# Kernel optimization log

Measured on AMD Instinct MI355X. Metric: run time of the kernel, lower is better.

## Reference

```python
import jax, jax.numpy as jnp
import numpy as np

N_KERNELS = 21
N_LAYERS = 2
N_HEADS = 8
ATT_DIM = 32
FF_HID = 100
EMB = 300


def kernel_mus(n):
    mus = [1.0]
    bin_size = 2.0 / (n - 1)
    mus.append(1.0 - bin_size / 2.0)
    for _ in range(1, n - 1):
        mus.append(mus[-1] - bin_size)
    return np.array(mus, dtype=np.float32)


def kernel_sigmas(n):
    return np.array([0.001] + [0.1] * (n - 1), dtype=np.float32)


def setup_inputs() -> dict:
    key = jax.random.key(0)
    ks = jax.random.split(key, 12)
    B, LQ, LD = 32, 64, 512
    u = lambda k, s, a: jax.random.uniform(k, s, jnp.float32, -a, a)
    return dict(
        q_embed=jax.random.normal(ks[0], (B, LQ, EMB), jnp.float32),
        d_embed=jax.random.normal(ks[1], (B, LD, EMB), jnp.float32),
        mask_q=(jax.random.uniform(ks[2], (B, LQ)) > 0.1).astype(jnp.float32),
        mask_d=(jax.random.uniform(ks[3], (B, LD)) > 0.1).astype(jnp.float32),
        mixer=jnp.full((1, 1, 1), 0.5, jnp.float32),
        nn_scaler=jnp.full((1,), 0.01, jnp.float32),
        ff_w1=u(ks[4], (N_LAYERS, EMB, FF_HID), 0.05),
        ff_b1=jnp.zeros((N_LAYERS, FF_HID), jnp.float32),
        ff_w2=u(ks[5], (N_LAYERS, FF_HID, EMB), 0.05),
        ff_b2=jnp.zeros((N_LAYERS, EMB), jnp.float32),
        ln1_g=jnp.ones((N_LAYERS, EMB), jnp.float32),
        ln1_b=jnp.zeros((N_LAYERS, EMB), jnp.float32),
        att_w=u(ks[6], (N_LAYERS, EMB, 3 * ATT_DIM), 0.05),
        att_b=jnp.zeros((N_LAYERS, 3 * ATT_DIM), jnp.float32),
        out_w=u(ks[7], (N_LAYERS, ATT_DIM, EMB), 0.05),
        out_b=jnp.zeros((N_LAYERS, EMB), jnp.float32),
        ln2_g=jnp.ones((N_LAYERS, EMB), jnp.float32),
        ln2_b=jnp.zeros((N_LAYERS, EMB), jnp.float32),
        dense_w=u(ks[8], (1, N_KERNELS), 0.014),
    )


def _layer_norm(x, g, b, eps=1e-6):
    m = jnp.mean(x, -1, keepdims=True)
    s = jnp.std(x, -1, keepdims=True, ddof=1)  # torch std is unbiased
    return g * (x - m) / (s + eps) + b


def _encoder(x, mask, p):
    # AllenNLP StackedSelfAttentionEncoder: [FF -> res+LN -> MHSA -> res+LN] x2
    B, T, E = x.shape
    scale = jnp.sqrt(jnp.float32(E // N_HEADS))
    hd = ATT_DIM // N_HEADS
    for l in range(N_LAYERS):
        h = jax.nn.relu(x @ p['ff_w1'][l] + p['ff_b1'][l]) @ p['ff_w2'][l] + p['ff_b2'][l]
        h = _layer_norm(h + x, p['ln1_g'][l], p['ln1_b'][l])
        c = h @ p['att_w'][l] + p['att_b'][l]              # [B,T,3*ATT_DIM]
        q = c[..., :ATT_DIM].reshape(B, T, N_HEADS, hd)
        k = c[..., ATT_DIM:2 * ATT_DIM].reshape(B, T, N_HEADS, hd)
        v = c[..., 2 * ATT_DIM:].reshape(B, T, N_HEADS, hd)
        sims = jnp.einsum('bqhd,bkhd->bhqk', q / scale, k)
        m = mask[:, None, None, :]
        att = jax.nn.softmax(sims * m, axis=-1) * m         # AllenNLP masked_softmax
        att = att / (jnp.sum(att, -1, keepdims=True) + 1e-13)
        o = jnp.einsum('bhqk,bkhd->bqhd', att, v).reshape(B, T, ATT_DIM)
        o = o @ p['out_w'][l] + p['out_b'][l]
        x = _layer_norm(o + h, p['ln2_g'][l], p['ln2_b'][l])
    return x


def reference(q_embed, d_embed, mask_q, mask_d, mixer, nn_scaler,
              ff_w1, ff_b1, ff_w2, ff_b2, ln1_g, ln1_b,
              att_w, att_b, out_w, out_b, ln2_g, ln2_b, dense_w):
    p = dict(ff_w1=ff_w1, ff_b1=ff_b1, ff_w2=ff_w2, ff_b2=ff_b2,
             ln1_g=ln1_g, ln1_b=ln1_b, att_w=att_w, att_b=att_b,
             out_w=out_w, out_b=out_b, ln2_g=ln2_g, ln2_b=ln2_b)
    mu = jnp.asarray(kernel_mus(N_KERNELS))        # [K]
    sigma = jnp.asarray(kernel_sigmas(N_KERNELS))  # [K]
    mq = mask_q[..., None]
    md = mask_d[..., None]
    q = q_embed * mq
    d = d_embed * md
    qc = _encoder(q, mask_q, p)
    dc = _encoder(d, mask_d, p)
    q = (mixer * q + (1.0 - mixer) * qc) * mq
    d = (mixer * d + (1.0 - mixer) * dc) * md
    qd_mask = mask_q[:, :, None] * mask_d[:, None, :]  # [B,Q,D]
    qn = q / (jnp.linalg.norm(q, axis=-1, keepdims=True) + 1e-13)
    dn = d / (jnp.linalg.norm(d, axis=-1, keepdims=True) + 1e-13)
    cos = jnp.einsum('bqe,bde->bqd', qn, dn) * qd_mask
    # Gaussian RBF soft histogram: [B,Q,D,K]
    kr = jnp.exp(-(cos[..., None] - mu) ** 2 / (2.0 * sigma ** 2)) * qd_mask[..., None]
    pkq = jnp.sum(kr, axis=2)                                 # [B,Q,K]
    log_pkq = jnp.log2(jnp.clip(pkq, 1e-10)) * nn_scaler
    per_kernel = jnp.sum(log_pkq * mq, axis=1)                # [B,K]
    return jnp.squeeze(per_kernel @ dense_w.T, axis=1)        # [B]
```

## Files before the change

### kernel.cpp

```cpp
#include <hip/hip_runtime.h>
#include <hip/hip_bf16.h>

#define BATCH 32
#define LQ 64
#define LD 512
#define EMB 300
#define FFH 100
#define ATTD 32
#define NH 8
#define NK 21
#define MQ (BATCH * LQ)
#define MD (BATCH * LD)
#define MALL (MQ + MD)

typedef __attribute__((ext_vector_type(8))) short bf16x8;
typedef __attribute__((ext_vector_type(4))) float f32x4;

__device__ __forceinline__ float wave_sum(float v) {
    #pragma unroll
    for (int off = 32; off > 0; off >>= 1) v += __shfl_xor(v, off);
    return v;
}

__device__ __forceinline__ float bf2f(__hip_bfloat16 h) {
    return __bfloat162float(h);
}

__device__ __forceinline__ float4 bf4_to_f4(const __hip_bfloat16* p) {
    uint2 u = *(const uint2*)p;
    float4 f;
    f.x = __uint_as_float((u.x & 0xffffu) << 16);
    f.y = __uint_as_float(u.x & 0xffff0000u);
    f.z = __uint_as_float((u.y & 0xffffu) << 16);
    f.w = __uint_as_float(u.y & 0xffff0000u);
    return f;
}

__global__ void maskmul_all(const float* __restrict__ q_embed, const float* __restrict__ d_embed,
                            const float* __restrict__ mask_q, const float* __restrict__ mask_d,
                            __hip_bfloat16* __restrict__ xbf, float* __restrict__ mall) {
    int i = blockIdx.x * blockDim.x + threadIdx.x;
    if (i >= MALL * EMB) return;
    int tok = i / EMB;
    float m, v;
    if (tok < MQ) {
        m = mask_q[tok];
        v = q_embed[i];
    } else {
        m = mask_d[tok - MQ];
        v = d_embed[i - MQ * EMB];
    }
    xbf[i] = __float2bfloat16(v * m);
    if (i % EMB == 0) mall[tok] = m;
}

__device__ __forceinline__ void conv_seg(const float* __restrict__ w, __hip_bfloat16* __restrict__ wt,
                                         int j, int K, int N) {
    int l = j / (K * N);
    int r = j % (K * N);
    int k = r / N, n = r % N;
    wt[(size_t)l * N * K + (size_t)n * K + k] = __float2bfloat16(w[j]);
}
__global__ void convert_all(const float* __restrict__ w1, const float* __restrict__ w2,
                            const float* __restrict__ aw, const float* __restrict__ ow,
                            __hip_bfloat16* __restrict__ w1t, __hip_bfloat16* __restrict__ w2t,
                            __hip_bfloat16* __restrict__ awt, __hip_bfloat16* __restrict__ owt) {
    int i = blockIdx.x * blockDim.x + threadIdx.x;
    const int S1 = 2 * EMB * FFH;
    const int S2 = S1 + 2 * FFH * EMB;
    const int S3 = S2 + 2 * EMB * 96;
    const int S4 = S3 + 2 * ATTD * EMB;
    if (i < S1)       conv_seg(w1, w1t, i, EMB, FFH);
    else if (i < S2)  conv_seg(w2, w2t, i - S1, FFH, EMB);
    else if (i < S3)  conv_seg(aw, awt, i - S2, EMB, 96);
    else if (i < S4)  conv_seg(ow, owt, i - S3, ATTD, EMB);
}

__device__ __forceinline__ void stage_row8(const __hip_bfloat16* __restrict__ src, bool rowvalid,
                                           int K, int gk, __hip_bfloat16* dst) {
    if (rowvalid && gk + 8 <= K) {
        const uint2* p = (const uint2*)(src + gk);
        uint2 a = p[0], b = p[1];
        *(uint2*)dst = a;
        *(uint2*)(dst + 4) = b;
    } else {
        #pragma unroll
        for (int j = 0; j < 8; j++)
            dst[j] = (rowvalid && gk + j < K) ? src[gk + j] : __float2bfloat16(0.f);
    }
}

template <bool RELU, bool HAS_RES>
__global__ __launch_bounds__(256) void gemm_mfma(const __hip_bfloat16* __restrict__ A,
                                                 const __hip_bfloat16* __restrict__ Bt,
                                                 const float* __restrict__ bias,
                                                 const __hip_bfloat16* __restrict__ Rres,
                                                 __hip_bfloat16* __restrict__ Cb,
                                                 int M, int N, int K) {
    __shared__ __align__(16) __hip_bfloat16 As[64][40];
    __shared__ __align__(16) __hip_bfloat16 Bs[64][40];
    const int tid = threadIdx.x;
    const int m0 = blockIdx.y * 64, n0 = blockIdx.x * 64;
    const int lane = tid & 63;
    const int wv = tid >> 6;
    const int wm = wv >> 1, wn = wv & 1;
    const int l15 = lane & 15, lg = lane >> 4;
    const int srow = tid >> 2, sk8 = (tid & 3) * 8;
    f32x4 acc[2][2] = {};
    const int NS = (K + 31) >> 5;
    const __hip_bfloat16* arow = A + (size_t)(m0 + srow) * K;
    const bool bvalid = (n0 + srow) < N;
    const __hip_bfloat16* brow = Bt + (size_t)(n0 + srow) * K;

    for (int s = 0; s < NS; s++) {
        const int gk = (s << 5) + sk8;
        if (s) __syncthreads();
        stage_row8(arow, true, K, gk, &As[srow][sk8]);
        stage_row8(brow, bvalid, K, gk, &Bs[srow][sk8]);
        __syncthreads();
        bf16x8 af0 = *(const bf16x8*)&As[wm * 32 + l15][lg * 8];
        bf16x8 af1 = *(const bf16x8*)&As[wm * 32 + 16 + l15][lg * 8];
        bf16x8 bf0 = *(const bf16x8*)&Bs[wn * 32 + l15][lg * 8];
        bf16x8 bf1 = *(const bf16x8*)&Bs[wn * 32 + 16 + l15][lg * 8];
        acc[0][0] = __builtin_amdgcn_mfma_f32_16x16x32_bf16(af0, bf0, acc[0][0], 0, 0, 0);
        acc[0][1] = __builtin_amdgcn_mfma_f32_16x16x32_bf16(af0, bf1, acc[0][1], 0, 0, 0);
        acc[1][0] = __builtin_amdgcn_mfma_f32_16x16x32_bf16(af1, bf0, acc[1][0], 0, 0, 0);
        acc[1][1] = __builtin_amdgcn_mfma_f32_16x16x32_bf16(af1, bf1, acc[1][1], 0, 0, 0);
    }

    #pragma unroll
    for (int fc = 0; fc < 2; fc++) {
        int col = n0 + wn * 32 + fc * 16 + l15;
        if (col >= N) continue;
        float bs = bias[col];
        #pragma unroll
        for (int fr = 0; fr < 2; fr++) {
            int rbase = m0 + wm * 32 + fr * 16 + lg * 4;
            #pragma unroll
            for (int r = 0; r < 4; r++) {
                int row = rbase + r;
                float v = acc[fr][fc][r] + bs;
                if (RELU) v = fmaxf(v, 0.f);
                size_t idx = (size_t)row * N + col;
                if (HAS_RES) v += bf2f(Rres[idx]);
                Cb[idx] = __float2bfloat16(v);
            }
        }
    }
}

__global__ __launch_bounds__(256) void cos_mfma(const __hip_bfloat16* __restrict__ Qn,
                                                const __hip_bfloat16* __restrict__ Dn,
                                                float* __restrict__ Cos) {
    __shared__ __align__(16) __hip_bfloat16 As[64][40];
    __shared__ __align__(16) __hip_bfloat16 Bs[64][40];
    const int b = blockIdx.y;
    const int n0 = blockIdx.x * 64;
    const int tid = threadIdx.x;
    const int lane = tid & 63;
    const int wv = tid >> 6;
    const int wm = wv >> 1, wn = wv & 1;
    const int l15 = lane & 15, lg = lane >> 4;
    const int srow = tid >> 2, sk8 = (tid & 3) * 8;
    f32x4 acc[2][2] = {};
    const int NS = (EMB + 31) >> 5;
    const __hip_bfloat16* arow = Qn + ((size_t)b * LQ + srow) * EMB;
    const __hip_bfloat16* brow = Dn + ((size_t)b * LD + n0 + srow) * EMB;

    for (int s = 0; s < NS; s++) {
        const int gk = (s << 5) + sk8;
        if (s) __syncthreads();
        stage_row8(arow, true, EMB, gk, &As[srow][sk8]);
        stage_row8(brow, true, EMB, gk, &Bs[srow][sk8]);
        __syncthreads();
        bf16x8 af0 = *(const bf16x8*)&As[wm * 32 + l15][lg * 8];
        bf16x8 af1 = *(const bf16x8*)&As[wm * 32 + 16 + l15][lg * 8];
        bf16x8 bf0 = *(const bf16x8*)&Bs[wn * 32 + l15][lg * 8];
        bf16x8 bf1 = *(const bf16x8*)&Bs[wn * 32 + 16 + l15][lg * 8];
        acc[0][0] = __builtin_amdgcn_mfma_f32_16x16x32_bf16(af0, bf0, acc[0][0], 0, 0, 0);
        acc[0][1] = __builtin_amdgcn_mfma_f32_16x16x32_bf16(af0, bf1, acc[0][1], 0, 0, 0);
        acc[1][0] = __builtin_amdgcn_mfma_f32_16x16x32_bf16(af1, bf0, acc[1][0], 0, 0, 0);
        acc[1][1] = __builtin_amdgcn_mfma_f32_16x16x32_bf16(af1, bf1, acc[1][1], 0, 0, 0);
    }

    float* cb = Cos + (size_t)b * LQ * LD;
    #pragma unroll
    for (int fc = 0; fc < 2; fc++) {
        int col = n0 + wn * 32 + fc * 16 + l15;
        #pragma unroll
        for (int fr = 0; fr < 2; fr++) {
            int rbase = wm * 32 + fr * 16 + lg * 4;
            #pragma unroll
            for (int r = 0; r < 4; r++) {
                cb[(size_t)(rbase + r) * LD + col] = acc[fr][fc][r];
            }
        }
    }
}

__global__ __launch_bounds__(256) void ln_bf(const __hip_bfloat16* __restrict__ X,
                                             const float* __restrict__ g,
                                             const float* __restrict__ bta,
                                             __hip_bfloat16* __restrict__ Y, int M) {
    int wid = (blockIdx.x * 256 + threadIdx.x) >> 6;
    int lane = threadIdx.x & 63;
    if (wid >= M) return;
    const __hip_bfloat16* x = X + (size_t)wid * EMB;
    float v[5];
    float s = 0.f;
    #pragma unroll
    for (int r = 0; r < 5; r++) {
        int idx = lane + r * 64;
        float val = (idx < EMB) ? bf2f(x[idx]) : 0.f;
        v[r] = val;
        s += val;
    }
    s = wave_sum(s);
    float mean = s * (1.f / EMB);
    float s2 = 0.f;
    #pragma unroll
    for (int r = 0; r < 5; r++) {
        int idx = lane + r * 64;
        if (idx < EMB) { float d = v[r] - mean; s2 += d * d; }
    }
    s2 = wave_sum(s2);
    float stdv = sqrtf(s2 * (1.f / (EMB - 1)));
    float inv = 1.f / (stdv + 1e-6f);
    __hip_bfloat16* y = Y + (size_t)wid * EMB;
    #pragma unroll
    for (int r = 0; r < 5; r++) {
        int idx = lane + r * 64;
        if (idx < EMB) y[idx] = __float2bfloat16(g[idx] * (v[r] - mean) * inv + bta[idx]);
    }
}

template <int T, int RPB, int KS>
__global__ __launch_bounds__(512) void attn_fused(const __hip_bfloat16* __restrict__ c,
                                                  const float* __restrict__ mask,
                                                  __hip_bfloat16* __restrict__ o32) {
    constexpr int BLK = RPB * KS;
    constexpr int NRB = T / RPB;
    __shared__ float4 Ks[T];
    __shared__ float4 Vs[T];
    __shared__ float part[RPB * 5 * (KS - 1)];
    __shared__ float nmask_s;
    const int bh = blockIdx.x / NRB;
    const int rb = blockIdx.x % NRB;
    const int b = bh / NH, h = bh % NH;
    const int tid = threadIdx.x;
    const __hip_bfloat16* base = c + (size_t)b * T * 96;

    if (tid == 0) nmask_s = 0.f;
    __syncthreads();
    float lnm = 0.f;
    for (int j = tid; j < T; j += BLK) {
        float m = mask[b * T + j];
        float4 kv = bf4_to_f4(base + (size_t)j * 96 + ATTD + h * 4);
        float4 vv = bf4_to_f4(base + (size_t)j * 96 + 2 * ATTD + h * 4);
        kv.x *= m; kv.y *= m; kv.z *= m; kv.w *= m;
        vv.x *= m; vv.y *= m; vv.z *= m; vv.w *= m;
        Ks[j] = kv;
        Vs[j] = vv;
        lnm += 1.f - m;
    }
    lnm = wave_sum(lnm);
    if ((tid & 63) == 0 && lnm != 0.f) atomicAdd(&nmask_s, lnm);
    __syncthreads();

    const int r = rb * RPB + (tid % RPB);
    const int ks = tid / RPB;
    const float inv_scale = 0.16439898730535729f;
    float4 qv = bf4_to_f4(base + (size_t)r * 96 + h * 4);
    qv.x *= inv_scale; qv.y *= inv_scale; qv.z *= inv_scale; qv.w *= inv_scale;

    float Sall = 0.f, ox = 0.f, oy = 0.f, oz = 0.f, ow = 0.f;
    constexpr int KC = T / KS;
    const int k0 = ks * KC;
    #pragma unroll 4
    for (int k = k0; k < k0 + KC; k++) {
        float4 kv = Ks[k];
        float4 vv = Vs[k];
        float s = fmaf(qv.x, kv.x, fmaf(qv.y, kv.y, fmaf(qv.z, kv.z, qv.w * kv.w)));
        float e = __expf(s);
        Sall += e;
        ox = fmaf(e, vv.x, ox);
        oy = fmaf(e, vv.y, oy);
        oz = fmaf(e, vv.z, oz);
        ow = fmaf(e, vv.w, ow);
    }
    if (ks > 0) {
        float* p = &part[((ks - 1) * RPB + (tid % RPB)) * 5];
        p[0] = Sall; p[1] = ox; p[2] = oy; p[3] = oz; p[4] = ow;
    }
    __syncthreads();
    if (ks == 0) {
        #pragma unroll
        for (int s2 = 0; s2 < KS - 1; s2++) {
            const float* p = &part[(s2 * RPB + r - rb * RPB) * 5];
            Sall += p[0]; ox += p[1]; oy += p[2]; oz += p[3]; ow += p[4];
        }
        float Sm = Sall - nmask_s;
        float inv = 1.f / (Sm + 1e-13f * Sall);
        __hip_bfloat16* op = o32 + (size_t)(b * T + r) * ATTD + h * 4;
        op[0] = __float2bfloat16(ox * inv);
        op[1] = __float2bfloat16(oy * inv);
        op[2] = __float2bfloat16(oz * inv);
        op[3] = __float2bfloat16(ow * inv);
    }
}

__global__ __launch_bounds__(256) void mixnorm_bf(const __hip_bfloat16* __restrict__ x,
                                                  const __hip_bfloat16* __restrict__ xc,
                                                  const float* __restrict__ mask,
                                                  const float* __restrict__ mixer,
                                                  __hip_bfloat16* __restrict__ out) {
    int wid = (blockIdx.x * 256 + threadIdx.x) >> 6;
    int lane = threadIdx.x & 63;
    float mixv = mixer[0];
    float mval = mask[wid];
    const __hip_bfloat16* xr = x + (size_t)wid * EMB;
    const __hip_bfloat16* xcr = xc + (size_t)wid * EMB;
    float v[5];
    float s2 = 0.f;
    #pragma unroll
    for (int r = 0; r < 5; r++) {
        int idx = lane + r * 64;
        float val = 0.f;
        if (idx < EMB) val = (mixv * bf2f(xr[idx]) + (1.f - mixv) * bf2f(xcr[idx])) * mval;
        v[r] = val;
        s2 += val * val;
    }
    s2 = wave_sum(s2);
    float inv = 1.f / (sqrtf(s2) + 1e-13f);
    __hip_bfloat16* o = out + (size_t)wid * EMB;
    #pragma unroll
    for (int r = 0; r < 5; r++) {
        int idx = lane + r * 64;
        if (idx < EMB) o[idx] = __float2bfloat16(v[r] * inv);
    }
}

__global__ __launch_bounds__(256) void pool_kernel(const float* __restrict__ Cos,
                                                   const float* __restrict__ mask_q,
                                                   const float* __restrict__ mask_d,
                                                   const float* __restrict__ nn_scaler,
                                                   float* __restrict__ lp) {
    int wid = (blockIdx.x * 256 + threadIdx.x) >> 6;
    int lane = threadIdx.x & 63;
    int b = wid >> 6, qi = wid & 63;
    const float* crow = Cos + ((size_t)b * LQ + qi) * LD;
    const float* md = mask_d + b * LD;
    float acc[NK];
    #pragma unroll
    for (int k = 0; k < NK; k++) acc[k] = 0.f;
    #pragma unroll
    for (int rr = 0; rr < LD / 64; rr++) {
        int dj = rr * 64 + lane;
        float m = md[dj];
        if (m != 0.f) {
            float cv = crow[dj];
            float d0 = cv - 1.0f;
            acc[0] += __expf(d0 * d0 * -500000.0f);
            #pragma unroll
            for (int g = 0; g < 4; g++) {
                float mu_a = 0.95f - 0.5f * g;
                float dc = cv - mu_a;
                float t = __expf(dc * dc * -50.0f);
                float r = __expf(fmaf(-10.0f, dc, -0.5f));
                #pragma unroll
                for (int j = 0; j < 5; j++) {
                    acc[1 + 5 * g + j] += t;
                    t *= r;
                    r *= 0.36787944117144233f;
                }
            }
        }
    }
    float mq = mask_q[b * LQ + qi];
    float ns = nn_scaler[0];
    #pragma unroll
    for (int k = 0; k < NK; k++) {
        float s = wave_sum(acc[k]);
        if (lane == 0) lp[((size_t)b * LQ + qi) * NK + k] = log2f(fmaxf(s, 1e-10f)) * ns * mq;
    }
}

__global__ void final_kernel(const float* __restrict__ lp, const float* __restrict__ dense_w,
                             float* __restrict__ out) {
    int b = blockIdx.x;
    int t = threadIdx.x;
    float s = 0.f;
    if (t < NK) {
        for (int qi = 0; qi < LQ; qi++) s += lp[((size_t)b * LQ + qi) * NK + t];
        s *= dense_w[t];
    }
    s = wave_sum(s);
    if (t == 0) out[b] = s;
}

extern "C" void kernel_launch(void* const* d_in, const int* in_sizes, int n_in,
                              void* d_out, int out_size, void* d_ws, size_t ws_size,
                              hipStream_t stream) {
    (void)in_sizes; (void)n_in; (void)out_size; (void)ws_size;
    const float* q_embed  = (const float*)d_in[0];
    const float* d_embed  = (const float*)d_in[1];
    const float* mask_q   = (const float*)d_in[2];
    const float* mask_d   = (const float*)d_in[3];
    const float* mixer    = (const float*)d_in[4];
    const float* nn_scaler= (const float*)d_in[5];
    const float* ff_w1    = (const float*)d_in[6];
    const float* ff_b1    = (const float*)d_in[7];
    const float* ff_w2    = (const float*)d_in[8];
    const float* ff_b2    = (const float*)d_in[9];
    const float* ln1_g    = (const float*)d_in[10];
    const float* ln1_b    = (const float*)d_in[11];
    const float* att_w    = (const float*)d_in[12];
    const float* att_b    = (const float*)d_in[13];
    const float* out_w    = (const float*)d_in[14];
    const float* out_b    = (const float*)d_in[15];
    const float* ln2_g    = (const float*)d_in[16];
    const float* ln2_b    = (const float*)d_in[17];
    const float* dense_w  = (const float*)d_in[18];
    float* out = (float*)d_out;

    float* ws   = (float*)d_ws;
    float* cosb = ws;
    float* lp   = cosb + 1048576;
    float* mall = lp + 43008;
    __hip_bfloat16* xbf   = (__hip_bfloat16*)(mall + MALL);
    __hip_bfloat16* xcbf  = xbf  + (size_t)MALL * EMB;
    __hip_bfloat16* xc2bf = xcbf + (size_t)MALL * EMB;
    __hip_bfloat16* t2bf  = xc2bf + (size_t)MALL * EMB;
    __hip_bfloat16* hbf   = t2bf + (size_t)MALL * EMB;
    __hip_bfloat16* t1bf  = hbf  + (size_t)MALL * EMB;
    __hip_bfloat16* cbf   = t1bf + (size_t)MALL * FFH;
    __hip_bfloat16* o32bf = cbf  + (size_t)MALL * 96;
    __hip_bfloat16* w1t   = o32bf + (size_t)MALL * ATTD;
    __hip_bfloat16* w2t   = w1t + 2 * FFH * EMB;
    __hip_bfloat16* awt   = w2t + 2 * EMB * FFH;
    __hip_bfloat16* owt   = awt + 2 * 96 * EMB;

    convert_all<<<(196800 + 255) / 256, 256, 0, stream>>>(ff_w1, ff_w2, att_w, out_w,
                                                          w1t, w2t, awt, owt);
    maskmul_all<<<(MALL * EMB + 255) / 256, 256, 0, stream>>>(q_embed, d_embed, mask_q, mask_d,
                                                              xbf, mall);

    const __hip_bfloat16* xcur = xbf;
    for (int l = 0; l < 2; l++) {
        __hip_bfloat16* xout = (l == 0) ? xcbf : xc2bf;
        gemm_mfma<true, false><<<dim3(2, MALL / 64), 256, 0, stream>>>(
            xcur, w1t + (size_t)l * FFH * EMB, ff_b1 + l * FFH, nullptr,
            t1bf, MALL, FFH, EMB);
        gemm_mfma<false, true><<<dim3(5, MALL / 64), 256, 0, stream>>>(
            t1bf, w2t + (size_t)l * EMB * FFH, ff_b2 + l * EMB, xcur,
            t2bf, MALL, EMB, FFH);
        ln_bf<<<MALL / 4, 256, 0, stream>>>(t2bf, ln1_g + l * EMB, ln1_b + l * EMB, hbf, MALL);
        gemm_mfma<false, false><<<dim3(2, MALL / 64), 256, 0, stream>>>(
            hbf, awt + (size_t)l * 96 * EMB, att_b + l * 96, nullptr,
            cbf, MALL, 96, EMB);
        attn_fused<LQ, 64, 8><<<BATCH * NH, 512, 0, stream>>>(cbf, mask_q, o32bf);
        attn_fused<LD, 128, 4><<<BATCH * NH * (LD / 128), 512, 0, stream>>>(
            cbf + (size_t)MQ * 96, mask_d, o32bf + (size_t)MQ * ATTD);
        gemm_mfma<false, true><<<dim3(5, MALL / 64), 256, 0, stream>>>(
            o32bf, owt + (size_t)l * EMB * ATTD, out_b + l * EMB, hbf,
            t2bf, MALL, EMB, ATTD);
        ln_bf<<<MALL / 4, 256, 0, stream>>>(t2bf, ln2_g + l * EMB, ln2_b + l * EMB, xout, MALL);
        xcur = xout;
    }

    mixnorm_bf<<<MALL / 4, 256, 0, stream>>>(xbf, xc2bf, mall, mixer, hbf);

    cos_mfma<<<dim3(LD / 64, BATCH), 256, 0, stream>>>(hbf, hbf + (size_t)MQ * EMB, cosb);

    pool_kernel<<<(BATCH * LQ) / 4, 256, 0, stream>>>(cosb, mask_q, mask_d, nn_scaler, lp);

    final_kernel<<<BATCH, 64, 0, stream>>>(lp, dense_w, out);
}
```

Baseline: 242.8 us.

## Fuse residual+LayerNorm into full-row GEMM epilogue and merge attention launches

```diff
diff --git a/kernel.cpp b/kernel.cpp
--- a/kernel.cpp
+++ b/kernel.cpp
@@ -90,11 +90,10 @@
     }
 }
 
-template <bool RELU, bool HAS_RES>
+template <bool RELU>
 __global__ __launch_bounds__(256) void gemm_mfma(const __hip_bfloat16* __restrict__ A,
                                                  const __hip_bfloat16* __restrict__ Bt,
                                                  const float* __restrict__ bias,
-                                                 const __hip_bfloat16* __restrict__ Rres,
                                                  __hip_bfloat16* __restrict__ Cb,
                                                  int M, int N, int K) {
     __shared__ __align__(16) __hip_bfloat16 As[64][40];
@@ -141,11 +140,250 @@
                 int row = rbase + r;
                 float v = acc[fr][fc][r] + bs;
                 if (RELU) v = fmaxf(v, 0.f);
-                size_t idx = (size_t)row * N + col;
-                if (HAS_RES) v += bf2f(Rres[idx]);
-                Cb[idx] = __float2bfloat16(v);
-            }
-        }
+                Cb[(size_t)row * N + col] = __float2bfloat16(v);
+            }
+        }
+    }
+}
+
+__global__ __launch_bounds__(256) void gemm_ln(const __hip_bfloat16* __restrict__ A,
+                                               const __hip_bfloat16* __restrict__ Bt,
+                                               const float* __restrict__ bias,
+                                               const __hip_bfloat16* __restrict__ Res,
+                                               const float* __restrict__ g,
+                                               const float* __restrict__ beta,
+                                               __hip_bfloat16* __restrict__ Y,
+                                               int M, int K) {
+    __shared__ __align__(16) __hip_bfloat16 As[32][40];
+    __shared__ __align__(16) __hip_bfloat16 Bs[320][40];
+    __shared__ float red[2][4][32];
+    const int tid = threadIdx.x;
+    const int m0 = blockIdx.x * 32;
+    const int lane = tid & 63;
+    const int wv = tid >> 6;
+    const int l15 = lane & 15, lg = lane >> 4;
+    const int c0 = wv * 80;
+    f32x4 acc[2][5] = {};
+    const int NS = (K + 31) >> 5;
+
+    for (int s = 0; s < NS; s++) {
+        const int gk0 = s << 5;
+        if (s) __syncthreads();
+        for (int ch = tid; ch < 1408; ch += 256) {
+            if (ch < 128) {
+                int row = ch >> 2, k8 = (ch & 3) * 8;
+                stage_row8(A + (size_t)(m0 + row) * K, true, K, gk0 + k8, &As[row][k8]);
+            } else {
+                int cc = ch - 128;
+                int row = cc >> 2, k8 = (cc & 3) * 8;
+                stage_row8(Bt + (size_t)row * K, row < EMB, K, gk0 + k8, &Bs[row][k8]);
+            }
+        }
+        __syncthreads();
+        bf16x8 af[2], bfr[5];
+        af[0] = *(const bf16x8*)&As[l15][lg * 8];
+        af[1] = *(const bf16x8*)&As[16 + l15][lg * 8];
+        #pragma unroll
+        for (int fc = 0; fc < 5; fc++)
+            bfr[fc] = *(const bf16x8*)&Bs[c0 + fc * 16 + l15][lg * 8];
+        #pragma unroll
+        for (int fr = 0; fr < 2; fr++)
+            #pragma unroll
+            for (int fc = 0; fc < 5; fc++)
+                acc[fr][fc] = __builtin_amdgcn_mfma_f32_16x16x32_bf16(af[fr], bfr[fc], acc[fr][fc], 0, 0, 0);
+    }
+
+    float rs[2][4];
+    #pragma unroll
+    for (int fr = 0; fr < 2; fr++)
+        #pragma unroll
+        for (int r = 0; r < 4; r++) rs[fr][r] = 0.f;
+    #pragma unroll
+    for (int fc = 0; fc < 5; fc++) {
+        int col = c0 + fc * 16 + l15;
+        bool valid = col < EMB;
+        float bs = valid ? bias[col] : 0.f;
+        #pragma unroll
+        for (int fr = 0; fr < 2; fr++) {
+            int rowb = m0 + fr * 16 + lg * 4;
+            #pragma unroll
+            for (int r = 0; r < 4; r++) {
+                float v = 0.f;
+                if (valid) v = acc[fr][fc][r] + bs + bf2f(Res[(size_t)(rowb + r) * EMB + col]);
+                acc[fr][fc][r] = v;
+                rs[fr][r] += v;
+            }
+        }
+    }
+    #pragma unroll
+    for (int fr = 0; fr < 2; fr++)
+        #pragma unroll
+        for (int r = 0; r < 4; r++)
+            #pragma unroll
+            for (int off = 1; off < 16; off <<= 1)
+                rs[fr][r] += __shfl_xor(rs[fr][r], off);
+    if (l15 == 0) {
+        #pragma unroll
+        for (int fr = 0; fr < 2; fr++)
+            #pragma unroll
+            for (int r = 0; r < 4; r++)
+                red[0][wv][fr * 16 + lg * 4 + r] = rs[fr][r];
+    }
+    __syncthreads();
+    float mean[2][4];
+    #pragma unroll
+    for (int fr = 0; fr < 2; fr++)
+        #pragma unroll
+        for (int r = 0; r < 4; r++) {
+            int ri = fr * 16 + lg * 4 + r;
+            mean[fr][r] = (red[0][0][ri] + red[0][1][ri] + red[0][2][ri] + red[0][3][ri]) * (1.f / EMB);
+        }
+    float rq[2][4];
+    #pragma unroll
+    for (int fr = 0; fr < 2; fr++)
+        #pragma unroll
+        for (int r = 0; r < 4; r++) rq[fr][r] = 0.f;
+    #pragma unroll
+    for (int fc = 0; fc < 5; fc++) {
+        int col = c0 + fc * 16 + l15;
+        bool valid = col < EMB;
+        #pragma unroll
+        for (int fr = 0; fr < 2; fr++)
+            #pragma unroll
+            for (int r = 0; r < 4; r++) {
+                if (valid) {
+                    float d = acc[fr][fc][r] - mean[fr][r];
+                    rq[fr][r] += d * d;
+                }
+            }
+    }
+    #pragma unroll
+    for (int fr = 0; fr < 2; fr++)
+        #pragma unroll
+        for (int r = 0; r < 4; r++)
+            #pragma unroll
+            for (int off = 1; off < 16; off <<= 1)
+                rq[fr][r] += __shfl_xor(rq[fr][r], off);
+    if (l15 == 0) {
+        #pragma unroll
+        for (int fr = 0; fr < 2; fr++)
+            #pragma unroll
+            for (int r = 0; r < 4; r++)
+                red[1][wv][fr * 16 + lg * 4 + r] = rq[fr][r];
+    }
+    __syncthreads();
+    float inv[2][4];
+    #pragma unroll
+    for (int fr = 0; fr < 2; fr++)
+        #pragma unroll
+        for (int r = 0; r < 4; r++) {
+            int ri = fr * 16 + lg * 4 + r;
+            float tot = red[1][0][ri] + red[1][1][ri] + red[1][2][ri] + red[1][3][ri];
+            float stdv = sqrtf(tot * (1.f / (EMB - 1)));
+            inv[fr][r] = 1.f / (stdv + 1e-6f);
+        }
+    #pragma unroll
+    for (int fc = 0; fc < 5; fc++) {
+        int col = c0 + fc * 16 + l15;
+        if (col >= EMB) continue;
+        float gv = g[col], bv = beta[col];
+        #pragma unroll
+        for (int fr = 0; fr < 2; fr++) {
+            int rowb = m0 + fr * 16 + lg * 4;
+            #pragma unroll
+            for (int r = 0; r < 4; r++) {
+                float y = gv * (acc[fr][fc][r] - mean[fr][r]) * inv[fr][r] + bv;
+                Y[(size_t)(rowb + r) * EMB + col] = __float2bfloat16(y);
+            }
+        }
+    }
+}
+
+template <int T, int RPB, int KS>
+__device__ __forceinline__ void attn_body(const __hip_bfloat16* __restrict__ cseg,
+                                          const float* __restrict__ mask,
+                                          __hip_bfloat16* __restrict__ oseg,
+                                          int bh, int rb, char* smem) {
+    constexpr int BLK = 512;
+    float4* Ks = (float4*)smem;
+    float4* Vs = Ks + T;
+    float* part = (float*)(Vs + T);
+    float* nmask_s = part + RPB * 5 * (KS - 1);
+    const int b = bh / NH, h = bh % NH;
+    const int tid = threadIdx.x;
+    const __hip_bfloat16* base = cseg + (size_t)b * T * 96;
+
+    if (tid == 0) *nmask_s = 0.f;
+    __syncthreads();
+    float lnm = 0.f;
+    for (int j = tid; j < T; j += BLK) {
+        float m = mask[b * T + j];
+        float4 kv = bf4_to_f4(base + (size_t)j * 96 + ATTD + h * 4);
+        float4 vv = bf4_to_f4(base + (size_t)j * 96 + 2 * ATTD + h * 4);
+        kv.x *= m; kv.y *= m; kv.z *= m; kv.w *= m;
+        vv.x *= m; vv.y *= m; vv.z *= m; vv.w *= m;
+        Ks[j] = kv;
+        Vs[j] = vv;
+        lnm += 1.f - m;
+    }
+    lnm = wave_sum(lnm);
+    if ((tid & 63) == 0 && lnm != 0.f) atomicAdd(nmask_s, lnm);
+    __syncthreads();
+
+    const int r = rb * RPB + (tid % RPB);
+    const int ks = tid / RPB;
+    const float inv_scale = 0.16439898730535729f;
+    float4 qv = bf4_to_f4(base + (size_t)r * 96 + h * 4);
+    qv.x *= inv_scale; qv.y *= inv_scale; qv.z *= inv_scale; qv.w *= inv_scale;
+
+    float Sall = 0.f, ox = 0.f, oy = 0.f, oz = 0.f, ow = 0.f;
+    constexpr int KC = T / KS;
+    const int k0 = ks * KC;
+    #pragma unroll 4
+    for (int k = k0; k < k0 + KC; k++) {
+        float4 kv = Ks[k];
+        float4 vv = Vs[k];
+        float s = fmaf(qv.x, kv.x, fmaf(qv.y, kv.y, fmaf(qv.z, kv.z, qv.w * kv.w)));
+        float e = __expf(s);
+        Sall += e;
+        ox = fmaf(e, vv.x, ox);
+        oy = fmaf(e, vv.y, oy);
+        oz = fmaf(e, vv.z, oz);
+        ow = fmaf(e, vv.w, ow);
+    }
+    if (ks > 0) {
+        float* p = &part[((ks - 1) * RPB + (tid % RPB)) * 5];
+        p[0] = Sall; p[1] = ox; p[2] = oy; p[3] = oz; p[4] = ow;
+    }
+    __syncthreads();
+    if (ks == 0) {
+        #pragma unroll
+        for (int s2 = 0; s2 < KS - 1; s2++) {
+            const float* p = &part[(s2 * RPB + r - rb * RPB) * 5];
+            Sall += p[0]; ox += p[1]; oy += p[2]; oz += p[3]; ow += p[4];
+        }
+        float Sm = Sall - *nmask_s;
+        float inv = 1.f / (Sm + 1e-13f * Sall);
+        __hip_bfloat16* op = oseg + (size_t)(b * T + r) * ATTD + h * 4;
+        op[0] = __float2bfloat16(ox * inv);
+        op[1] = __float2bfloat16(oy * inv);
+        op[2] = __float2bfloat16(oz * inv);
+        op[3] = __float2bfloat16(ow * inv);
+    }
+}
+
+__global__ __launch_bounds__(512) void attn_both(const __hip_bfloat16* __restrict__ cbf,
+                                                 const float* __restrict__ mask_q,
+                                                 const float* __restrict__ mask_d,
+                                                 __hip_bfloat16* __restrict__ o32) {
+    __shared__ __align__(16) char smem[24576];
+    int blk = blockIdx.x;
+    if (blk < BATCH * NH) {
+        attn_body<LQ, 64, 8>(cbf, mask_q, o32, blk, 0, smem);
+    } else {
+        int bid = blk - BATCH * NH;
+        attn_body<LD, 128, 4>(cbf + (size_t)MQ * 96, mask_d, o32 + (size_t)MQ * ATTD,
+                              bid >> 2, bid & 3, smem);
     }
 }
 
@@ -195,117 +433,6 @@
                 cb[(size_t)(rbase + r) * LD + col] = acc[fr][fc][r];
             }
         }
-    }
-}
-
-__global__ __launch_bounds__(256) void ln_bf(const __hip_bfloat16* __restrict__ X,
-                                             const float* __restrict__ g,
-                                             const float* __restrict__ bta,
-                                             __hip_bfloat16* __restrict__ Y, int M) {
-    int wid = (blockIdx.x * 256 + threadIdx.x) >> 6;
-    int lane = threadIdx.x & 63;
-    if (wid >= M) return;
-    const __hip_bfloat16* x = X + (size_t)wid * EMB;
-    float v[5];
-    float s = 0.f;
-    #pragma unroll
-    for (int r = 0; r < 5; r++) {
-        int idx = lane + r * 64;
-        float val = (idx < EMB) ? bf2f(x[idx]) : 0.f;
-        v[r] = val;
-        s += val;
-    }
-    s = wave_sum(s);
-    float mean = s * (1.f / EMB);
-    float s2 = 0.f;
-    #pragma unroll
-    for (int r = 0; r < 5; r++) {
-        int idx = lane + r * 64;
-        if (idx < EMB) { float d = v[r] - mean; s2 += d * d; }
-    }
-    s2 = wave_sum(s2);
-    float stdv = sqrtf(s2 * (1.f / (EMB - 1)));
-    float inv = 1.f / (stdv + 1e-6f);
-    __hip_bfloat16* y = Y + (size_t)wid * EMB;
-    #pragma unroll
-    for (int r = 0; r < 5; r++) {
-        int idx = lane + r * 64;
-        if (idx < EMB) y[idx] = __float2bfloat16(g[idx] * (v[r] - mean) * inv + bta[idx]);
-    }
-}
-
-template <int T, int RPB, int KS>
-__global__ __launch_bounds__(512) void attn_fused(const __hip_bfloat16* __restrict__ c,
-                                                  const float* __restrict__ mask,
-                                                  __hip_bfloat16* __restrict__ o32) {
-    constexpr int BLK = RPB * KS;
-    constexpr int NRB = T / RPB;
-    __shared__ float4 Ks[T];
-    __shared__ float4 Vs[T];
-    __shared__ float part[RPB * 5 * (KS - 1)];
-    __shared__ float nmask_s;
-    const int bh = blockIdx.x / NRB;
-    const int rb = blockIdx.x % NRB;
-    const int b = bh / NH, h = bh % NH;
-    const int tid = threadIdx.x;
-    const __hip_bfloat16* base = c + (size_t)b * T * 96;
-
-    if (tid == 0) nmask_s = 0.f;
-    __syncthreads();
-    float lnm = 0.f;
-    for (int j = tid; j < T; j += BLK) {
-        float m = mask[b * T + j];
-        float4 kv = bf4_to_f4(base + (size_t)j * 96 + ATTD + h * 4);
-        float4 vv = bf4_to_f4(base + (size_t)j * 96 + 2 * ATTD + h * 4);
-        kv.x *= m; kv.y *= m; kv.z *= m; kv.w *= m;
-        vv.x *= m; vv.y *= m; vv.z *= m; vv.w *= m;
-        Ks[j] = kv;
-        Vs[j] = vv;
-        lnm += 1.f - m;
-    }
-    lnm = wave_sum(lnm);
-    if ((tid & 63) == 0 && lnm != 0.f) atomicAdd(&nmask_s, lnm);
-    __syncthreads();
-
-    const int r = rb * RPB + (tid % RPB);
-    const int ks = tid / RPB;
-    const float inv_scale = 0.16439898730535729f;
-    float4 qv = bf4_to_f4(base + (size_t)r * 96 + h * 4);
-    qv.x *= inv_scale; qv.y *= inv_scale; qv.z *= inv_scale; qv.w *= inv_scale;
-
-    float Sall = 0.f, ox = 0.f, oy = 0.f, oz = 0.f, ow = 0.f;
-    constexpr int KC = T / KS;
-    const int k0 = ks * KC;
-    #pragma unroll 4
-    for (int k = k0; k < k0 + KC; k++) {
-        float4 kv = Ks[k];
-        float4 vv = Vs[k];
-        float s = fmaf(qv.x, kv.x, fmaf(qv.y, kv.y, fmaf(qv.z, kv.z, qv.w * kv.w)));
-        float e = __expf(s);
-        Sall += e;
-        ox = fmaf(e, vv.x, ox);
-        oy = fmaf(e, vv.y, oy);
-        oz = fmaf(e, vv.z, oz);
-        ow = fmaf(e, vv.w, ow);
-    }
-    if (ks > 0) {
-        float* p = &part[((ks - 1) * RPB + (tid % RPB)) * 5];
-        p[0] = Sall; p[1] = ox; p[2] = oy; p[3] = oz; p[4] = ow;
-    }
-    __syncthreads();
-    if (ks == 0) {
-        #pragma unroll
-        for (int s2 = 0; s2 < KS - 1; s2++) {
-            const float* p = &part[(s2 * RPB + r - rb * RPB) * 5];
-            Sall += p[0]; ox += p[1]; oy += p[2]; oz += p[3]; ow += p[4];
-        }
-        float Sm = Sall - nmask_s;
-        float inv = 1.f / (Sm + 1e-13f * Sall);
-        __hip_bfloat16* op = o32 + (size_t)(b * T + r) * ATTD + h * 4;
-        op[0] = __float2bfloat16(ox * inv);
-        op[1] = __float2bfloat16(oy * inv);
-        op[2] = __float2bfloat16(oz * inv);
-        op[3] = __float2bfloat16(ow * inv);
     }
 }
 
@@ -430,8 +557,7 @@
     __hip_bfloat16* xbf   = (__hip_bfloat16*)(mall + MALL);
     __hip_bfloat16* xcbf  = xbf  + (size_t)MALL * EMB;
     __hip_bfloat16* xc2bf = xcbf + (size_t)MALL * EMB;
-    __hip_bfloat16* t2bf  = xc2bf + (size_t)MALL * EMB;
-    __hip_bfloat16* hbf   = t2bf + (size_t)MALL * EMB;
+    __hip_bfloat16* hbf   = xc2bf + (size_t)MALL * EMB;
     __hip_bfloat16* t1bf  = hbf  + (size_t)MALL * EMB;
     __hip_bfloat16* cbf   = t1bf + (size_t)MALL * FFH;
     __hip_bfloat16* o32bf = cbf  + (size_t)MALL * 96;
@@ -448,23 +574,18 @@
     const __hip_bfloat16* xcur = xbf;
     for (int l = 0; l < 2; l++) {
         __hip_bfloat16* xout = (l == 0) ? xcbf : xc2bf;
-        gemm_mfma<true, false><<<dim3(2, MALL / 64), 256, 0, stream>>>(
-            xcur, w1t + (size_t)l * FFH * EMB, ff_b1 + l * FFH, nullptr,
-            t1bf, MALL, FFH, EMB);
-        gemm_mfma<false, true><<<dim3(5, MALL / 64), 256, 0, stream>>>(
+        gemm_mfma<true><<<dim3(2, MALL / 64), 256, 0, stream>>>(
+            xcur, w1t + (size_t)l * FFH * EMB, ff_b1 + l * FFH, t1bf, MALL, FFH, EMB);
+        gemm_ln<<<MALL / 32, 256, 0, stream>>>(
             t1bf, w2t + (size_t)l * EMB * FFH, ff_b2 + l * EMB, xcur,
-            t2bf, MALL, EMB, FFH);
-        ln_bf<<<MALL / 4, 256, 0, stream>>>(t2bf, ln1_g + l * EMB, ln1_b + l * EMB, hbf, MALL);
-        gemm_mfma<false, false><<<dim3(2, MALL / 64), 256, 0, stream>>>(
-            hbf, awt + (size_t)l * 96 * EMB, att_b + l * 96, nullptr,
-            cbf, MALL, 96, EMB);
-        attn_fused<LQ, 64, 8><<<BATCH * NH, 512, 0, stream>>>(cbf, mask_q, o32bf);
-        attn_fused<LD, 128, 4><<<BATCH * NH * (LD / 128), 512, 0, stream>>>(
-            cbf + (size_t)MQ * 96, mask_d, o32bf + (size_t)MQ * ATTD);
-        gemm_mfma<false, true><<<dim3(5, MALL / 64), 256, 0, stream>>>(
+            ln1_g + l * EMB, ln1_b + l * EMB, hbf, MALL, FFH);
+        gemm_mfma<false><<<dim3(2, MALL / 64), 256, 0, stream>>>(
+            hbf, awt + (size_t)l * 96 * EMB, att_b + l * 96, cbf, MALL, 96, EMB);
+        attn_both<<<BATCH * NH + BATCH * NH * (LD / 128), 512, 0, stream>>>(
+            cbf, mask_q, mask_d, o32bf);
+        gemm_ln<<<MALL / 32, 256, 0, stream>>>(
             o32bf, owt + (size_t)l * EMB * ATTD, out_b + l * EMB, hbf,
-            t2bf, MALL, EMB, ATTD);
-        ln_bf<<<MALL / 4, 256, 0, stream>>>(t2bf, ln2_g + l * EMB, ln2_b + l * EMB, xout, MALL);
+            ln2_g + l * EMB, ln2_b + l * EMB, xout, MALL, ATTD);
         xcur = xout;
     }
 
```

After: 242.5 us. About the same (-0.1%).
